# Performance work log

Hardware: AMD Instinct MI355X
Metric: run time of the kernel (lower is better)

## Reference

```python
import jax, jax.numpy as jnp
import numpy as np

N_ENT = 100000
N_REL = 12
D = 64
E = 1000000
LAYER_DIMS = [64, 32]


def _xavier(key, shape):
    fan_in, fan_out = shape[-1], shape[-2] if len(shape) >= 2 else shape[-1]
    std = np.sqrt(2.0 / (fan_in + fan_out)).astype(np.float32)
    return jax.random.normal(key, shape, jnp.float32) * std


def setup_inputs() -> dict:
    key = jax.random.key(0)
    ks = jax.random.split(key, 14)
    return {
        "entity_emb": _xavier(ks[0], (N_ENT, D)),
        "rel_emb": _xavier(ks[1], (N_REL, D)),
        "W_r": _xavier(ks[2], (N_REL, D, D)),
        "W1_0_w": _xavier(ks[3], (LAYER_DIMS[0], D)),
        "W1_0_b": jnp.zeros((LAYER_DIMS[0],), jnp.float32),
        "W2_0_w": _xavier(ks[4], (LAYER_DIMS[0], D)),
        "W2_0_b": jnp.zeros((LAYER_DIMS[0],), jnp.float32),
        "W1_1_w": _xavier(ks[5], (LAYER_DIMS[1], LAYER_DIMS[0])),
        "W1_1_b": jnp.zeros((LAYER_DIMS[1],), jnp.float32),
        "W2_1_w": _xavier(ks[6], (LAYER_DIMS[1], LAYER_DIMS[0])),
        "W2_1_b": jnp.zeros((LAYER_DIMS[1],), jnp.float32),
        "src": jax.random.randint(ks[7], (E,), 0, N_ENT, jnp.int32),
        "dst": jax.random.randint(ks[8], (E,), 0, N_ENT, jnp.int32),
        "etype": jax.random.randint(ks[9], (E,), 0, N_REL, jnp.int32),
    }


def reference(entity_emb, rel_emb, W_r, W1_0_w, W1_0_b, W2_0_w, W2_0_b,
              W1_1_w, W1_1_b, W2_1_w, W2_1_b, src, dst, etype):
    n = entity_emb.shape[0]

    # --- compute_attention: per-edge TransR scores, edge_softmax over dst ---
    # Instead of gathering W_r[etype] per edge ([E,D,D] is huge), project every
    # node by every relation matrix once: [N, R, Dr].
    proj = jnp.einsum('nd,kdr->nkr', entity_emb, W_r)
    tail = proj[src, etype]          # [E, Dr] (src projected by its edge's W_r)
    head = proj[dst, etype]          # [E, Dr]
    rel = rel_emb[etype]             # [E, Dr]
    logits = jnp.sum(tail * jnp.tanh(head + rel), axis=-1)  # [E]

    # edge softmax grouped by destination node (stable)
    m = jax.ops.segment_max(logits, dst, num_segments=n)
    ex = jnp.exp(logits - m[dst])
    den = jax.ops.segment_sum(ex, dst, num_segments=n)
    att = ex / den[dst]              # [E]

    # --- KGATLayer: gather-scale-scatter + bi-interaction (dropout = 0) ---
    def layer(x, W1w, W1b, W2w, W2b):
        h_n = jax.ops.segment_sum(x[src] * att[:, None], dst, num_segments=n)
        add = jax.nn.leaky_relu((x + h_n) @ W1w.T + W1b)
        mul = jax.nn.leaky_relu((x * h_n) @ W2w.T + W2b)
        return add + mul

    x0 = entity_emb
    x1 = layer(x0, W1_0_w, W1_0_b, W2_0_w, W2_0_b)
    x2 = layer(x1, W1_1_w, W1_1_b, W2_1_w, W2_1_b)
    # embedder concatenates the input and every layer output
    return jnp.concatenate([x0, x1, x2], axis=1)  # [N, 64+64+32]
```

## Files before the change

kernel.cpp:

```cpp
#include <hip/hip_runtime.h>
#include <hip/hip_bf16.h>
#include <math.h>


typedef __attribute__((ext_vector_type(8))) short short8;
typedef __attribute__((ext_vector_type(4))) float float4v;

__device__ __forceinline__ short f2bf(float f) {
  __hip_bfloat16 h = __float2bfloat16(f);
  return *(short*)&h;
}
__device__ __forceinline__ float bf2f(short s) {
  return __uint_as_float(((unsigned)(unsigned short)s) << 16);
}

#define LOG2E 1.4426950408889634f
#define BS1_TILE 2048

__global__ void k_prep(const float* __restrict__ emb, short* __restrict__ emb_h,
                       float* __restrict__ out,
                       const float* __restrict__ Wr, short* __restrict__ Bt,
                       const float* __restrict__ W10, const float* __restrict__ W20,
                       const float* __restrict__ W11, const float* __restrict__ W21,
                       short* __restrict__ w1h0, short* __restrict__ w1l0,
                       short* __restrict__ w2h0, short* __restrict__ w2l0,
                       short* __restrict__ w1h1, short* __restrict__ w1l1,
                       short* __restrict__ w2h1, short* __restrict__ w2l1,
                       const int* __restrict__ src, const int* __restrict__ dst,
                       const int* __restrict__ et, int* __restrict__ bcur,
                       uint2* __restrict__ stg, int nE, int bsh, int cap,
                       int nb1, int nb_cvt, int n4) {
  __shared__ int hist[256];
  __shared__ int base[256];
  int b = blockIdx.x, t = threadIdx.x;
  if (b < nb1) {
    hist[t] = 0;
    __syncthreads();
    int tile = b * BS1_TILE;
#pragma unroll
    for (int j = 0; j < BS1_TILE / 256; j++) {
      int e = tile + j * 256 + t;
      if (e < nE) atomicAdd(&hist[dst[e] >> bsh], 1);
    }
    __syncthreads();
    int cnt = hist[t];
    if (cnt > 0) base[t] = atomicAdd(&bcur[t], cnt);
    hist[t] = 0;
    __syncthreads();
#pragma unroll
    for (int j = 0; j < BS1_TILE / 256; j++) {
      int e = tile + j * 256 + t;
      if (e < nE) {
        int d = dst[e], bk = d >> bsh;
        int r = atomicAdd(&hist[bk], 1);
        stg[(size_t)bk * cap + base[bk] + r] =
            make_uint2((unsigned)src[e], (unsigned)d | ((unsigned)et[e] << 20));
      }
    }
    return;
  }
  int b2 = b - nb1;
  if (b2 < nb_cvt) {
    int i = b2 * 256 + t;
    if (i < n4) {
      float4 v = ((const float4*)emb)[i];
      union { short s[4]; uint2 u; } o;
      o.s[0] = f2bf(v.x); o.s[1] = f2bf(v.y); o.s[2] = f2bf(v.z); o.s[3] = f2bf(v.w);
      ((uint2*)emb_h)[i] = o.u;
      int node = i >> 4, ch = i & 15;
      *(float4*)(out + (size_t)node * 160 + ch * 4) = v;
    }
  } else if (b2 < nb_cvt + 12) {
    int k = b2 - nb_cvt;
    for (int i = t; i < 4096; i += 256) {
      int d = i >> 6, r = i & 63;
      Bt[k * 4096 + r * 64 + d] = f2bf(Wr[k * 4096 + i]);
    }
  } else {
    int i = (b2 - nb_cvt - 12) * 256 + t;
    const float* W; short* H; short* L; int j;
    if (i < 4096) { W = W10; H = w1h0; L = w1l0; j = i; }
    else if (i < 8192) { W = W20; H = w2h0; L = w2l0; j = i - 4096; }
    else if (i < 10240) { W = W11; H = w1h1; L = w1l1; j = i - 8192; }
    else if (i < 12288) { W = W21; H = w2h1; L = w2l1; j = i - 10240; }
    else return;
    float w = W[j];
    short hi = f2bf(w);
    H[j] = hi;
    L[j] = f2bf(w - bf2f(hi));
  }
}

__global__ __launch_bounds__(256) void k_projb2(const short* __restrict__ A,
                                                const short* __restrict__ Bt,
                                                short* __restrict__ proj,
                                                int n_ent,
                                                const uint2* __restrict__ stg,
                                                const int* __restrict__ bcur,
                                                int* __restrict__ row_ptr,
                                                uint2* __restrict__ csr2,
                                                int nbg, int bsh, int cap,
                                                int nbuck, int nE) {
  __shared__ char smem[4 * 64 * 72 * 2];
  int bid = blockIdx.x, t = threadIdx.x;
  if (bid >= nbg) {
    int b = bid - nbg;
    int* cnt = (int*)smem;
    int* sc = cnt + 1024;
    int* bs = sc + 1024;
    int v = (t < nbuck) ? bcur[t] : 0;
    bs[t] = v;
    __syncthreads();
    for (int o = 1; o < 256; o <<= 1) {
      int a = (t >= o) ? bs[t - o] : 0;
      __syncthreads();
      bs[t] += a;
      __syncthreads();
    }
    int gbase = bs[b] - bcur[b];
    int n = n_ent;
    int lo = b << bsh;
    if (lo > n) lo = n;
    int hi = (b + 1) << bsh;
    if (hi > n) hi = n;
    int w = hi - lo;
#pragma unroll
    for (int j = 0; j < 4; j++) cnt[t + j * 256] = 0;
    __syncthreads();
    int m = bcur[b];
    const uint2* S = stg + (size_t)b * cap;
    for (int p = t; p < m; p += 256)
      atomicAdd(&cnt[(int)(S[p].y & 0xFFFFFu) - lo], 1);
    __syncthreads();
#pragma unroll
    for (int j = 0; j < 4; j++) sc[t + j * 256] = cnt[t + j * 256];
    __syncthreads();
    for (int o = 1; o < 1024; o <<= 1) {
      int a[4];
#pragma unroll
      for (int j = 0; j < 4; j++) {
        int i = t + j * 256;
        a[j] = (i >= o) ? sc[i - o] : 0;
      }
      __syncthreads();
#pragma unroll
      for (int j = 0; j < 4; j++) sc[t + j * 256] += a[j];
      __syncthreads();
    }
#pragma unroll
    for (int j = 0; j < 4; j++) {
      int i = t + j * 256;
      if (i < w) {
        int c0 = gbase + sc[i] - cnt[i];
        row_ptr[lo + i] = c0;
        cnt[i] = c0;
      }
    }
    if (b == nbuck - 1 && t == 0) row_ptr[n] = nE;
    __syncthreads();
    for (int p = t; p < m; p += 256) {
      uint2 vv = S[p];
      int d = (int)(vv.y & 0xFFFFFu);
      int pos = atomicAdd(&cnt[d - lo], 1);
      csr2[pos] = vv;
    }
    return;
  }
  int wave = t >> 6, lane = t & 63;
  int quad = lane >> 4, l16 = lane & 15;
  int m0 = bid * 256 + wave * 64;
  unsigned short* W = (unsigned short*)smem + wave * 64 * 72;
  short8 a[4][2];
#pragma unroll
  for (int mt = 0; mt < 4; mt++)
#pragma unroll
    for (int kc = 0; kc < 2; kc++) {
      int row = m0 + mt * 16 + l16;
      int rr = row < n_ent ? row : 0;
      a[mt][kc] = *(const short8*)(A + (size_t)rr * 64 + kc * 32 + quad * 8);
    }
  for (int k = 0; k < 12; k++) {
    const short* B = Bt + k * 4096;
    short8 b[4][2];
#pragma unroll
    for (int nt = 0; nt < 4; nt++)
#pragma unroll
      for (int kc = 0; kc < 2; kc++)
        b[nt][kc] = *(const short8*)(B + (nt * 16 + l16) * 64 + kc * 32 + quad * 8);
    float4v acc[4][4];
#pragma unroll
    for (int mt = 0; mt < 4; mt++)
#pragma unroll
      for (int nt = 0; nt < 4; nt++)
        acc[mt][nt] = (float4v){0.f, 0.f, 0.f, 0.f};
#pragma unroll
    for (int kc = 0; kc < 2; kc++)
#pragma unroll
      for (int mt = 0; mt < 4; mt++)
#pragma unroll
        for (int nt = 0; nt < 4; nt++)
          acc[mt][nt] = __builtin_amdgcn_mfma_f32_16x16x32_bf16(
              a[mt][kc], b[nt][kc], acc[mt][nt], 0, 0, 0);
#pragma unroll
    for (int mt = 0; mt < 4; mt++)
#pragma unroll
      for (int nt = 0; nt < 4; nt++)
#pragma unroll
        for (int r = 0; r < 4; r++) {
          int row = mt * 16 + quad * 4 + r;
          int col = nt * 16 + l16;
          W[row * 72 + col] = (unsigned short)f2bf(acc[mt][nt][r]);
        }
    const size_t plane = (size_t)k * n_ent;
#pragma unroll
    for (int i = 0; i < 8; i++) {
      int row = (lane >> 3) + 8 * i;
      int cs = (lane & 7) * 8;
      short8 v = *(const short8*)(W + row * 72 + cs);
      int node = m0 + row;
      if (node < n_ent)
        *(short8*)(proj + (plane + node) * 64 + cs) = v;
    }
  }
}

__global__ __launch_bounds__(256) void k_logits(const short* __restrict__ ps,
                                                const float* __restrict__ rel_emb,
                                                uint2* csr2, int nE, int n_ent,
                                                int nwg) {
  int bid = blockIdx.x;
  int q = nwg >> 3, r8 = nwg & 7;
  int xcd = bid & 7, idx = bid >> 3;
  int swz = (xcd < r8 ? xcd * (q + 1) : r8 * (q + 1) + (xcd - r8) * q) + idx;
  int t = threadIdx.x;
  int lane = t & 63;
  int sub = lane >> 3;
  int c8 = (lane & 7) * 8;
  int e0 = (swz * 4 + (t >> 6)) * 64;
  if (e0 >= nE) return;
  int ku[8];
  short8 tl[8], hd[8];
#pragma unroll
  for (int u = 0; u < 8; u++) {
    int e = e0 + u * 8 + sub;
    int ee = e < nE ? e : nE - 1;
    uint2 c = csr2[ee];
    int s = (int)c.x;
    int d = (int)(c.y & 0xFFFFFu);
    int k = (int)(c.y >> 20);
    ku[u] = k;
    const size_t plane = (size_t)k * n_ent;
    tl[u] = *(const short8*)(ps + (plane + s) * 64 + c8);
    hd[u] = *(const short8*)(ps + (plane + d) * 64 + c8);
  }
  float v[8];
#pragma unroll
  for (int u = 0; u < 8; u++) {
    const float* rp = rel_emb + ku[u] * 64 + c8;
    float4 r0 = *(const float4*)rp;
    float4 r1 = *(const float4*)(rp + 4);
    float rr[8] = {r0.x, r0.y, r0.z, r0.w, r1.x, r1.y, r1.z, r1.w};
    float vv = 0.f;
#pragma unroll
    for (int qq = 0; qq < 8; qq++) {
      float x = bf2f(hd[u][qq]) + rr[qq];
      float tt = __builtin_amdgcn_exp2f(x * (2.f * LOG2E));
      float rc = __builtin_amdgcn_rcpf(tt + 1.f);
      float th = fmaf(-2.f, rc, 1.f);
      vv = fmaf(bf2f(tl[u][qq]), th, vv);
    }
    vv += __shfl_xor(vv, 1);
    vv += __shfl_xor(vv, 2);
    vv += __shfl_xor(vv, 4);
    v[u] = __builtin_amdgcn_exp2f(vv * LOG2E);
  }
  int uu = lane & 7;
  float myv = v[0];
#pragma unroll
  for (int u = 1; u < 8; u++)
    if (uu == u) myv = v[u];
  int e = e0 + uu * 8 + sub;
  if (e < nE) csr2[e].y = __float_as_uint(myv);
}

__global__ __launch_bounds__(256) void k_agg(const short* __restrict__ xh,
                                             const int* __restrict__ row_ptr,
                                             const uint2* __restrict__ csr,
                                             float* __restrict__ hn, int n_ent) {
  int wave = threadIdx.x >> 6, lane = threadIdx.x & 63;
  int n = blockIdx.x * 4 + wave;
  if (n >= n_ent) return;
  int jb = row_ptr[n], je = row_ptr[n + 1];
  int deg = je - jb;
  if (deg == 0) {
    hn[(size_t)n * 64 + lane] = 0.f;
    return;
  }
  uint2 c = (lane < deg) ? csr[jb + lane] : make_uint2(0u, 0u);
  int sidx = (int)c.x;
  float exv = (lane < deg) ? __uint_as_float(c.y) : 0.f;
  float den = exv;
#pragma unroll
  for (int o = 32; o; o >>= 1) den += __shfl_xor(den, o);
  int m = deg < 64 ? deg : 64;
  float acc = 0.f;
  for (int j = 0; j < m; j += 8) {
    int s0 = __shfl(sidx, j), s1 = __shfl(sidx, j + 1);
    int s2 = __shfl(sidx, j + 2), s3 = __shfl(sidx, j + 3);
    int s4 = __shfl(sidx, j + 4), s5 = __shfl(sidx, j + 5);
    int s6 = __shfl(sidx, j + 6), s7 = __shfl(sidx, j + 7);
    float e0 = __shfl(exv, j), e1 = __shfl(exv, j + 1);
    float e2 = __shfl(exv, j + 2), e3 = __shfl(exv, j + 3);
    float e4 = __shfl(exv, j + 4), e5 = __shfl(exv, j + 5);
    float e6 = __shfl(exv, j + 6), e7 = __shfl(exv, j + 7);
    short g0 = xh[(size_t)s0 * 64 + lane];
    short g1 = xh[(size_t)s1 * 64 + lane];
    short g2 = xh[(size_t)s2 * 64 + lane];
    short g3 = xh[(size_t)s3 * 64 + lane];
    short g4 = xh[(size_t)s4 * 64 + lane];
    short g5 = xh[(size_t)s5 * 64 + lane];
    short g6 = xh[(size_t)s6 * 64 + lane];
    short g7 = xh[(size_t)s7 * 64 + lane];
    acc = fmaf(e0, bf2f(g0), acc); acc = fmaf(e1, bf2f(g1), acc);
    acc = fmaf(e2, bf2f(g2), acc); acc = fmaf(e3, bf2f(g3), acc);
    acc = fmaf(e4, bf2f(g4), acc); acc = fmaf(e5, bf2f(g5), acc);
    acc = fmaf(e6, bf2f(g6), acc); acc = fmaf(e7, bf2f(g7), acc);
  }
  if (deg > 64) {
    for (int jj = jb + 64; jj < je; jj++) {
      uint2 cc = csr[jj];
      float ee = __uint_as_float(cc.y);
      den += ee;
      acc = fmaf(ee, bf2f(xh[(size_t)cc.x * 64 + lane]), acc);
    }
  }
  hn[(size_t)n * 64 + lane] = acc / den;
}

template <int OD, bool FIRST>
__global__ __launch_bounds__(256) void k_upmfma(const float* __restrict__ x,
                                                const float* __restrict__ hn,
                                                const short* __restrict__ g1h,
                                                const short* __restrict__ g1l,
                                                const short* __restrict__ g2h,
                                                const short* __restrict__ g2l,
                                                const float* __restrict__ b1,
                                                const float* __restrict__ b2,
                                                float* __restrict__ out,
                                                float* __restrict__ x_next,
                                                short* __restrict__ xh_next,
                                                int n_ent) {
  constexpr int NT = OD / 16;
  constexpr int S = (OD == 64) ? 66 : 34;
  __shared__ short wbuf[4 * OD * 72];
  short* w1h = wbuf;
  short* w1l = wbuf + OD * 72;
  short* w2h = wbuf + 2 * OD * 72;
  short* w2l = wbuf + 3 * OD * 72;
  int t = threadIdx.x;
  for (int i = t; i < OD * 16; i += 256) {
    int o = i >> 4, dq = (i & 15) * 4;
    *(uint2*)(w1h + o * 72 + dq) = *(const uint2*)(g1h + o * 64 + dq);
    *(uint2*)(w1l + o * 72 + dq) = *(const uint2*)(g1l + o * 64 + dq);
    *(uint2*)(w2h + o * 72 + dq) = *(const uint2*)(g2h + o * 64 + dq);
    *(uint2*)(w2l + o * 72 + dq) = *(const uint2*)(g2l + o * 64 + dq);
  }
  int wave = t >> 6, lane = t & 63;
  int quad = lane >> 4, l16 = lane & 15;
  int m0 = blockIdx.x * 128 + wave * 32;
  float4v accA[2][NT], accM[2][NT];
#pragma unroll
  for (int mt = 0; mt < 2; mt++)
#pragma unroll
    for (int nt = 0; nt < NT; nt++) {
      accA[mt][nt] = (float4v){0.f, 0.f, 0.f, 0.f};
      accM[mt][nt] = (float4v){0.f, 0.f, 0.f, 0.f};
    }
  __syncthreads();
#pragma unroll
  for (int kc = 0; kc < 2; kc++) {
    short8 ah_add[2], al_add[2], ah_mul[2], al_mul[2];
#pragma unroll
    for (int mt = 0; mt < 2; mt++) {
      int row = m0 + mt * 16 + l16;
      int rr = row < n_ent ? row : 0;
      const float* xp = x + (size_t)rr * 64 + kc * 32 + quad * 8;
      const float* hp = hn + (size_t)rr * 64 + kc * 32 + quad * 8;
      float4 xa = *(const float4*)xp;
      float4 xb = *(const float4*)(xp + 4);
      float4 ha = *(const float4*)hp;
      float4 hb = *(const float4*)(hp + 4);
      float xs[8] = {xa.x, xa.y, xa.z, xa.w, xb.x, xb.y, xb.z, xb.w};
      float hs[8] = {ha.x, ha.y, ha.z, ha.w, hb.x, hb.y, hb.z, hb.w};
#pragma unroll
      for (int qq = 0; qq < 8; qq++) {
        float s = xs[qq] + hs[qq];
        short shi = f2bf(s);
        ah_add[mt][qq] = shi;
        al_add[mt][qq] = f2bf(s - bf2f(shi));
        float p = xs[qq] * hs[qq];
        short phi = f2bf(p);
        ah_mul[mt][qq] = phi;
        al_mul[mt][qq] = f2bf(p - bf2f(phi));
      }
    }
#pragma unroll
    for (int nt = 0; nt < NT; nt++) {
      int boff = (nt * 16 + l16) * 72 + kc * 32 + quad * 8;
      short8 b1h = *(const short8*)(w1h + boff);
      short8 b1l = *(const short8*)(w1l + boff);
      short8 b2h = *(const short8*)(w2h + boff);
      short8 b2l = *(const short8*)(w2l + boff);
#pragma unroll
      for (int mt = 0; mt < 2; mt++) {
        accA[mt][nt] = __builtin_amdgcn_mfma_f32_16x16x32_bf16(
            ah_add[mt], b1h, accA[mt][nt], 0, 0, 0);
        accA[mt][nt] = __builtin_amdgcn_mfma_f32_16x16x32_bf16(
            al_add[mt], b1h, accA[mt][nt], 0, 0, 0);
        accA[mt][nt] = __builtin_amdgcn_mfma_f32_16x16x32_bf16(
            ah_add[mt], b1l, accA[mt][nt], 0, 0, 0);
        accM[mt][nt] = __builtin_amdgcn_mfma_f32_16x16x32_bf16(
            ah_mul[mt], b2h, accM[mt][nt], 0, 0, 0);
        accM[mt][nt] = __builtin_amdgcn_mfma_f32_16x16x32_bf16(
            al_mul[mt], b2h, accM[mt][nt], 0, 0, 0);
        accM[mt][nt] = __builtin_amdgcn_mfma_f32_16x16x32_bf16(
            ah_mul[mt], b2l, accM[mt][nt], 0, 0, 0);
      }
    }
  }
  __syncthreads();
  float* yt = (float*)wbuf + wave * 32 * S;
#pragma unroll
  for (int nt = 0; nt < NT; nt++) {
    int col = nt * 16 + l16;
    float bb1 = b1[col], bb2 = b2[col];
#pragma unroll
    for (int mt = 0; mt < 2; mt++) {
#pragma unroll
      for (int r = 0; r < 4; r++) {
        float aa = accA[mt][nt][r] + bb1;
        float mm = accM[mt][nt][r] + bb2;
        aa = aa > 0.f ? aa : 0.01f * aa;
        mm = mm > 0.f ? mm : 0.01f * mm;
        yt[(mt * 16 + quad * 4 + r) * S + col] = aa + mm;
      }
    }
  }
  constexpr int LPR = OD / 4;
  constexpr int RPI = 64 / LPR;
#pragma unroll
  for (int i = 0; i < 32 / RPI; i++) {
    int rloc = i * RPI + lane / LPR;
    int c4 = (lane % LPR) * 4;
    float4 v = *(const float4*)(yt + rloc * S + c4);
    int node = m0 + rloc;
    if (node < n_ent) {
      if constexpr (FIRST) {
        *(float4*)(out + (size_t)node * 160 + 64 + c4) = v;
        *(float4*)(x_next + (size_t)node * 64 + c4) = v;
        unsigned p0 = (unsigned)(unsigned short)f2bf(v.x) |
                      ((unsigned)(unsigned short)f2bf(v.y) << 16);
        unsigned p1 = (unsigned)(unsigned short)f2bf(v.z) |
                      ((unsigned)(unsigned short)f2bf(v.w) << 16);
        *(uint2*)(xh_next + (size_t)node * 64 + c4) = make_uint2(p0, p1);
      } else {
        *(float4*)(out + (size_t)node * 160 + 128 + c4) = v;
      }
    }
  }
}

extern "C" void kernel_launch(void* const* d_in, const int* in_sizes, int n_in,
                              void* d_out, int out_size, void* d_ws, size_t ws_size,
                              hipStream_t stream) {
  const float* emb = (const float*)d_in[0];
  const float* rel = (const float*)d_in[1];
  const float* Wr = (const float*)d_in[2];
  const float* W10w = (const float*)d_in[3];
  const float* W10b = (const float*)d_in[4];
  const float* W20w = (const float*)d_in[5];
  const float* W20b = (const float*)d_in[6];
  const float* W11w = (const float*)d_in[7];
  const float* W11b = (const float*)d_in[8];
  const float* W21w = (const float*)d_in[9];
  const float* W21b = (const float*)d_in[10];
  const int* src = (const int*)d_in[11];
  const int* dst = (const int*)d_in[12];
  const int* et = (const int*)d_in[13];
  int N = in_sizes[0] / 64;
  int E = in_sizes[11];
  float* out = (float*)d_out;

  int bsh = 9;
  while (((N + (1 << bsh) - 1) >> bsh) > 256) bsh++;
  int nbuck = (N + (1 << bsh) - 1) >> bsh;
  int cap = ((E / nbuck) * 3 / 2 + 1024 + 255) / 256 * 256;

  char* p = (char*)d_ws;
  auto alloc = [&](size_t bytes) -> char* {
    char* r = p;
    p += (bytes + 255) / 256 * 256;
    return r;
  };
  short* proj = (short*)alloc((size_t)N * 768 * 2);
  uint2* csr2 = (uint2*)alloc((size_t)E * 8);
  uint2* stg = (uint2*)alloc((size_t)nbuck * cap * 8);
  int* row_ptr = (int*)alloc((size_t)(N + 1) * 4);
  int* bcur = (int*)alloc(1024);
  float* hn = (float*)alloc((size_t)N * 64 * 4);
  float* x1 = (float*)alloc((size_t)N * 64 * 4);
  short* emb_h = (short*)alloc(((size_t)N + 256) * 64 * 2);
  short* x1h = (short*)alloc(((size_t)N + 256) * 64 * 2);
  short* Bt = (short*)alloc((size_t)12 * 4096 * 2);
  short* w1h0 = (short*)alloc(4096 * 2);
  short* w1l0 = (short*)alloc(4096 * 2);
  short* w2h0 = (short*)alloc(4096 * 2);
  short* w2l0 = (short*)alloc(4096 * 2);
  short* w1h1 = (short*)alloc(2048 * 2);
  short* w1l1 = (short*)alloc(2048 * 2);
  short* w2h1 = (short*)alloc(2048 * 2);
  short* w2l1 = (short*)alloc(2048 * 2);

  int n4 = N * 16;
  int nb_cvt = (n4 + 255) / 256;
  int nb1 = (E + BS1_TILE - 1) / BS1_TILE;
  int nbg = (N + 255) / 256;
  int nwg_lg = (E + 255) / 256;

  hipMemsetAsync(bcur, 0, 1024, stream);
  k_prep<<<nb1 + nb_cvt + 60, 256, 0, stream>>>(
      emb, emb_h, out, Wr, Bt, W10w, W20w, W11w, W21w,
      w1h0, w1l0, w2h0, w2l0, w1h1, w1l1, w2h1, w2l1,
      src, dst, et, bcur, stg, E, bsh, cap, nb1, nb_cvt, n4);
  k_projb2<<<nbg + nbuck, 256, 0, stream>>>(
      emb_h, Bt, proj, N, stg, bcur, row_ptr, csr2, nbg, bsh, cap, nbuck, E);
  k_logits<<<nwg_lg, 256, 0, stream>>>(proj, rel, csr2, E, N, nwg_lg);
  k_agg<<<(N + 3) / 4, 256, 0, stream>>>(emb_h, row_ptr, csr2, hn, N);
  k_upmfma<64, true><<<(N + 127) / 128, 256, 0, stream>>>(
      emb, hn, w1h0, w1l0, w2h0, w2l0, W10b, W20b, out, x1, x1h, N);
  k_agg<<<(N + 3) / 4, 256, 0, stream>>>(x1h, row_ptr, csr2, hn, N);
  k_upmfma<32, false><<<(N + 127) / 128, 256, 0, stream>>>(
      x1, hn, w1h1, w1l1, w2h1, w2l1, W11b, W21b, out, nullptr, nullptr, N);
}
```

Measured before the change: 335.6 us.

## Shrink projection/CSR blocks to 128 threads and rework bucket scans

The fused projection and CSR-build kernel now runs 128-thread blocks with half the shared memory, so twice as many GEMM blocks are launched and more blocks fit per CU. The CSR-bucket path replaces the 256-wide Hillis-Steele scan over bucket counts with a wave-shuffle reduction of the preceding buckets. It also replaces the 1024-wide shared scan with a per-thread serial scan of 8 counts plus a 128-wide double-buffered scan, cutting barriers. The risk is that fewer threads per bucket block slow the atomic histogram and scatter loops.

```diff
diff --git a/kernel.cpp b/kernel.cpp
--- a/kernel.cpp
+++ b/kernel.cpp
@@ -91,7 +91,7 @@
   }
 }
 
-__global__ __launch_bounds__(256) void k_projb2(const short* __restrict__ A,
+__global__ __launch_bounds__(128) void k_projb2(const short* __restrict__ A,
                                                 const short* __restrict__ Bt,
                                                 short* __restrict__ proj,
                                                 int n_ent,
@@ -101,64 +101,61 @@
                                                 uint2* __restrict__ csr2,
                                                 int nbg, int bsh, int cap,
                                                 int nbuck, int nE) {
-  __shared__ char smem[4 * 64 * 72 * 2];
+  __shared__ char smem[2 * 64 * 72 * 2];
   int bid = blockIdx.x, t = threadIdx.x;
   if (bid >= nbg) {
     int b = bid - nbg;
     int* cnt = (int*)smem;
-    int* sc = cnt + 1024;
-    int* bs = sc + 1024;
-    int v = (t < nbuck) ? bcur[t] : 0;
-    bs[t] = v;
-    __syncthreads();
-    for (int o = 1; o < 256; o <<= 1) {
-      int a = (t >= o) ? bs[t - o] : 0;
-      __syncthreads();
-      bs[t] += a;
-      __syncthreads();
-    }
-    int gbase = bs[b] - bcur[b];
+    int* ss = cnt + 1024;
+    int* red = ss + 256;
+    int v1 = (t < b) ? bcur[t] : 0;
+    int t2 = t + 128;
+    int v2 = (t2 < nbuck && t2 < b) ? bcur[t2] : 0;
+    int myv = v1 + v2;
+#pragma unroll
+    for (int o = 32; o; o >>= 1) myv += __shfl_xor(myv, o);
+    if ((t & 63) == 0) red[t >> 6] = myv;
+#pragma unroll
+    for (int j = 0; j < 8; j++) cnt[t + j * 128] = 0;
+    __syncthreads();
+    int gbase = red[0] + red[1];
     int n = n_ent;
     int lo = b << bsh;
     if (lo > n) lo = n;
     int hi = (b + 1) << bsh;
     if (hi > n) hi = n;
     int w = hi - lo;
-#pragma unroll
-    for (int j = 0; j < 4; j++) cnt[t + j * 256] = 0;
-    __syncthreads();
     int m = bcur[b];
     const uint2* S = stg + (size_t)b * cap;
-    for (int p = t; p < m; p += 256)
+    for (int p = t; p < m; p += 128)
       atomicAdd(&cnt[(int)(S[p].y & 0xFFFFFu) - lo], 1);
     __syncthreads();
-#pragma unroll
-    for (int j = 0; j < 4; j++) sc[t + j * 256] = cnt[t + j * 256];
-    __syncthreads();
-    for (int o = 1; o < 1024; o <<= 1) {
-      int a[4];
-#pragma unroll
-      for (int j = 0; j < 4; j++) {
-        int i = t + j * 256;
-        a[j] = (i >= o) ? sc[i - o] : 0;
-      }
+    int base_ = t * 8;
+    int loc[8], s = 0;
+#pragma unroll
+    for (int j = 0; j < 8; j++) { loc[j] = s; s += cnt[base_ + j]; }
+    int pp = 0;
+    ss[t] = s;
+    __syncthreads();
+    for (int o = 1; o < 128; o <<= 1) {
+      int a = (t >= o) ? ss[pp * 128 + t - o] : 0;
+      ss[(pp ^ 1) * 128 + t] = ss[pp * 128 + t] + a;
+      pp ^= 1;
       __syncthreads();
-#pragma unroll
-      for (int j = 0; j < 4; j++) sc[t + j * 256] += a[j];
-      __syncthreads();
-    }
-#pragma unroll
-    for (int j = 0; j < 4; j++) {
-      int i = t + j * 256;
+    }
+    int pre = gbase + ss[pp * 128 + t] - s;
+#pragma unroll
+    for (int j = 0; j < 8; j++) {
+      int i = base_ + j;
       if (i < w) {
-        int c0 = gbase + sc[i] - cnt[i];
+        int c0 = pre + loc[j];
         row_ptr[lo + i] = c0;
         cnt[i] = c0;
       }
     }
     if (b == nbuck - 1 && t == 0) row_ptr[n] = nE;
     __syncthreads();
-    for (int p = t; p < m; p += 256) {
+    for (int p = t; p < m; p += 128) {
       uint2 vv = S[p];
       int d = (int)(vv.y & 0xFFFFFu);
       int pos = atomicAdd(&cnt[d - lo], 1);
@@ -168,7 +165,7 @@
   }
   int wave = t >> 6, lane = t & 63;
   int quad = lane >> 4, l16 = lane & 15;
-  int m0 = bid * 256 + wave * 64;
+  int m0 = bid * 128 + wave * 64;
   unsigned short* W = (unsigned short*)smem + wave * 64 * 72;
   short8 a[4][2];
 #pragma unroll
@@ -524,7 +521,7 @@
   int n4 = N * 16;
   int nb_cvt = (n4 + 255) / 256;
   int nb1 = (E + BS1_TILE - 1) / BS1_TILE;
-  int nbg = (N + 255) / 256;
+  int nbg = (N + 127) / 128;
   int nwg_lg = (E + 255) / 256;
 
   hipMemsetAsync(bcur, 0, 1024, stream);
@@ -532,7 +529,7 @@
       emb, emb_h, out, Wr, Bt, W10w, W20w, W11w, W21w,
       w1h0, w1l0, w2h0, w2l0, w1h1, w1l1, w2h1, w2l1,
       src, dst, et, bcur, stg, E, bsh, cap, nb1, nb_cvt, n4);
-  k_projb2<<<nbg + nbuck, 256, 0, stream>>>(
+  k_projb2<<<nbg + nbuck, 128, 0, stream>>>(
       emb_h, Bt, proj, N, stg, bcur, row_ptr, csr2, nbg, bsh, cap, nbuck, E);
   k_logits<<<nwg_lg, 256, 0, stream>>>(proj, rel, csr2, E, N, nwg_lg);
   k_agg<<<(N + 3) / 4, 256, 0, stream>>>(emb_h, row_ptr, csr2, hn, N);
```

Measured after the change: 337.6 us. No clear change (+0.6%).
